# Performance work log

Hardware: AMD Instinct MI355X
Metric: run time of the kernel (lower is better)

## Reference

```python
import jax, jax.numpy as jnp
import numpy as np

ENC, TAG, LANG, ATT = 512, 512, 512, 256
N, P = 1024, 1024


def setup_inputs() -> dict:
    key = jax.random.key(0)
    ks = jax.random.split(key, 11)
    s = lambda d: 1.0 / np.sqrt(d)
    return {
        "encoder_out": jax.random.normal(ks[0], (1, P, ENC), jnp.float32),
        "decoder_hidden": jax.random.normal(ks[1], (N, TAG), jnp.float32),
        "language_out": jax.random.normal(ks[2], (N, LANG), jnp.float32),
        "We": jax.random.uniform(ks[3], (ATT, ENC), jnp.float32, -s(ENC), s(ENC)),
        "be": jax.random.uniform(ks[4], (ATT,), jnp.float32, -s(ENC), s(ENC)),
        "Wt": jax.random.uniform(ks[5], (ATT, TAG), jnp.float32, -s(TAG), s(TAG)),
        "bt": jax.random.uniform(ks[6], (ATT,), jnp.float32, -s(TAG), s(TAG)),
        "Wl": jax.random.uniform(ks[7], (ATT, LANG), jnp.float32, -s(LANG), s(LANG)),
        "bl": jax.random.uniform(ks[8], (ATT,), jnp.float32, -s(LANG), s(LANG)),
        "Wf": jax.random.uniform(ks[9], (1, ATT), jnp.float32, -s(ATT), s(ATT)),
        "bf": jax.random.uniform(ks[10], (1,), jnp.float32, -s(ATT), s(ATT)),
    }


def reference(encoder_out, decoder_hidden, language_out, We, be, Wt, bt, Wl, bl, Wf, bf):
    # att1: (1, P, A); att2, att3: (N, A)
    att1 = jnp.einsum("bpe,ae->bpa", encoder_out, We) + be
    att2 = decoder_hidden @ Wt.T + bt
    att3 = language_out @ Wl.T + bl
    # broadcast add -> (N, P, A), relu, reduce to scalar score per pixel
    h = jax.nn.relu(att1 + (att2 + att3)[:, None, :])  # (N, P, A)
    att = jnp.einsum("npa,a->np", h, Wf[0]) + bf[0]     # (N, P)
    alpha = jax.nn.softmax(att, axis=1)
    # softmax-weighted sum over pixels -> (N, ENC)
    awe = jnp.einsum("np,pe->ne", alpha, encoder_out[0])
    return awe, alpha
```

## Files before the change

### kernel.cpp

```cpp
#include <hip/hip_runtime.h>
#include <hip/hip_bf16.h>
#include <math.h>

#define ENC 512
#define ATT 256
#define NN 1024
#define PP 1024

typedef __attribute__((ext_vector_type(8))) __bf16 bf16x8;
typedef __attribute__((ext_vector_type(4))) float floatx4;
typedef __attribute__((ext_vector_type(2))) float floatx2;

union LdsVec { uint4 u; bf16x8 v; };

__device__ __forceinline__ unsigned cvt_pk(float lo, float hi) {
    union { __hip_bfloat162 h; unsigned u; } x;
    x.h = __float22bfloat162_rn(float2{lo, hi});
    return x.u;
}
__device__ __forceinline__ uint4 cvt8(float4 f0, float4 f1) {
    uint4 r;
    r.x = cvt_pk(f0.x, f0.y); r.y = cvt_pk(f0.z, f0.w);
    r.z = cvt_pk(f1.x, f1.y); r.w = cvt_pk(f1.z, f1.w);
    return r;
}

__device__ __forceinline__ int tile_off(int row, int k) {
    return row * 32 + ((((k >> 3) ^ ((row >> 1) & 3)) & 3) << 3) + (k & 7);
}

__device__ __forceinline__ void stage_bt(unsigned short* dst, const float* __restrict__ src,
                                         int ld, int k0, int tid) {
    const int row = tid >> 2, kseg = tid & 3;
    const float* p = src + (size_t)row * ld + k0 + kseg * 8;
    float4 f0 = *(const float4*)p;
    float4 f1 = *(const float4*)(p + 4);
    uint4 u = cvt8(f0, f1);
    *(uint4*)&dst[tile_off(row, kseg * 8)] = u;
}

__global__ __launch_bounds__(256) void mfma_uv(
    const float* __restrict__ E,  const float* __restrict__ We, const float* __restrict__ be,
    const float* __restrict__ D,  const float* __restrict__ Wt, const float* __restrict__ bt,
    const float* __restrict__ Lg, const float* __restrict__ Wl, const float* __restrict__ bl,
    float* __restrict__ uT, float* __restrict__ v1T, float* __restrict__ v2T,
    unsigned short* __restrict__ ET)
{
    const int tid = threadIdx.x;

    if (blockIdx.z == 3) {
        __shared__ unsigned short T[64][72];
        const int k0 = blockIdx.y * 64;
        const int kr = tid >> 2, nc = (tid & 3) * 16;
        const int nr = tid >> 2, kc = (tid & 3) * 16;
        #pragma unroll
        for (int t = 0; t < 2; ++t) {
            const int n0 = (blockIdx.x * 2 + t) * 64;
            const float* ep = E + (size_t)(k0 + kr) * ENC + n0 + nc;
            float4 a = *(const float4*)(ep + 0),  b = *(const float4*)(ep + 4);
            float4 c = *(const float4*)(ep + 8),  d = *(const float4*)(ep + 12);
            if (t) __syncthreads();
            *(uint4*)&T[kr][nc]     = cvt8(a, b);
            *(uint4*)&T[kr][nc + 8] = cvt8(c, d);
            __syncthreads();
            unsigned short tmp[16];
            #pragma unroll
            for (int i = 0; i < 16; ++i) tmp[i] = T[kc + i][nr];
            unsigned short* op = ET + (size_t)(n0 + nr) * PP + k0 + kc;
            *(uint4*)(op)     = *(uint4*)&tmp[0];
            *(uint4*)(op + 8) = *(uint4*)&tmp[8];
        }
        return;
    }

    __shared__ __align__(16) unsigned short As[2][64 * 32];
    __shared__ __align__(16) unsigned short Bs[2][64 * 32];
    const int K = 512;

    const float *A, *B, *bias; float* out;
    if      (blockIdx.z == 0) { A = E;  B = We; bias = be; out = uT;  }
    else if (blockIdx.z == 1) { A = D;  B = Wt; bias = bt; out = v1T; }
    else                      { A = Lg; B = Wl; bias = bl; out = v2T; }

    const int m0 = blockIdx.y * 64, n0 = blockIdx.x * 64;
    const int wv = tid >> 6, lm = tid & 15, lq = (tid >> 4) & 3;
    const int mb = (wv & 1) * 32, nb = (wv >> 1) * 32;
    const int a0o = tile_off(mb + lm,      lq * 8);
    const int a1o = tile_off(mb + 16 + lm, lq * 8);
    const int b0o = tile_off(nb + lm,      lq * 8);
    const int b1o = tile_off(nb + 16 + lm, lq * 8);

    const int row = tid >> 2, kseg = tid & 3;
    const int soff = tile_off(row, kseg * 8);
    const float* Ap = A + (size_t)(m0 + row) * K + kseg * 8;
    const float* Bp = B + (size_t)(n0 + row) * K + kseg * 8;

    floatx4 acc[2][2];
    const floatx4 zero = {0.f, 0.f, 0.f, 0.f};
    acc[0][0] = zero; acc[0][1] = zero; acc[1][0] = zero; acc[1][1] = zero;

    float4 pa0 = *(const float4*)(Ap), pa1 = *(const float4*)(Ap + 4);
    float4 pb0 = *(const float4*)(Bp), pb1 = *(const float4*)(Bp + 4);

    for (int k0 = 0; k0 < K; k0 += 32) {
        const int buf = (k0 >> 5) & 1;
        *(uint4*)&As[buf][soff] = cvt8(pa0, pa1);
        *(uint4*)&Bs[buf][soff] = cvt8(pb0, pb1);
        __syncthreads();
        if (k0 + 32 < K) {
            pa0 = *(const float4*)(Ap + k0 + 32); pa1 = *(const float4*)(Ap + k0 + 36);
            pb0 = *(const float4*)(Bp + k0 + 32); pb1 = *(const float4*)(Bp + k0 + 36);
        }
        LdsVec fa0, fa1, fb0, fb1;
        fa0.u = *(const uint4*)&As[buf][a0o];
        fa1.u = *(const uint4*)&As[buf][a1o];
        fb0.u = *(const uint4*)&Bs[buf][b0o];
        fb1.u = *(const uint4*)&Bs[buf][b1o];
        acc[0][0] = __builtin_amdgcn_mfma_f32_16x16x32_bf16(fa0.v, fb0.v, acc[0][0], 0, 0, 0);
        acc[0][1] = __builtin_amdgcn_mfma_f32_16x16x32_bf16(fa0.v, fb1.v, acc[0][1], 0, 0, 0);
        acc[1][0] = __builtin_amdgcn_mfma_f32_16x16x32_bf16(fa1.v, fb0.v, acc[1][0], 0, 0, 0);
        acc[1][1] = __builtin_amdgcn_mfma_f32_16x16x32_bf16(fa1.v, fb1.v, acc[1][1], 0, 0, 0);
    }

    #pragma unroll
    for (int s = 0; s < 2; ++s) {
        const int col = n0 + nb + s * 16 + lm;
        const float bsum = bias[col];
        #pragma unroll
        for (int t = 0; t < 2; ++t) {
            const int mbase = m0 + mb + t * 16 + lq * 4;
            float4 o;
            o.x = acc[t][s][0] + bsum; o.y = acc[t][s][1] + bsum;
            o.z = acc[t][s][2] + bsum; o.w = acc[t][s][3] + bsum;
            *(float4*)&out[(size_t)col * NN + mbase] = o;
        }
    }
}

__global__ __launch_bounds__(256) void att_fused(
    const float* __restrict__ uT, const float* __restrict__ v1T,
    const float* __restrict__ v2T,
    const float* __restrict__ Wf, float* __restrict__ att_part)
{
    __shared__ float us[32][68];
    __shared__ float vs[32][68];
    __shared__ float wfs[128];
    const int tid = threadIdx.x;
    const int z = blockIdx.z;
    if (tid < 128) wfs[tid] = Wf[z * 128 + tid];
    const int p0 = blockIdx.x * 64, n0 = blockIdx.y * 64;
    const int rowS = tid >> 3, cS = (tid & 7) * 8;
    const int tx = tid & 15, ty = tid >> 4;

    floatx2 acc[4][2];
    const floatx2 z2 = {0.f, 0.f};
    #pragma unroll
    for (int j = 0; j < 4; ++j) { acc[j][0] = z2; acc[j][1] = z2; }

    const int abase = z * 128;
    for (int ac = 0; ac < 128; ac += 32) {
        __syncthreads();
        {
            const float* up = &uT[(size_t)(abase + ac + rowS) * NN + p0 + cS];
            float4 f0 = *(const float4*)up;
            float4 f1 = *(const float4*)(up + 4);
            *(float4*)&us[rowS][cS]     = f0;
            *(float4*)&us[rowS][cS + 4] = f1;
            const size_t vidx = (size_t)(abase + ac + rowS) * NN + n0 + cS;
            float4 g0 = *(const float4*)&v1T[vidx];
            float4 g1 = *(const float4*)&v1T[vidx + 4];
            float4 h0 = *(const float4*)&v2T[vidx];
            float4 h1 = *(const float4*)&v2T[vidx + 4];
            float4 s0, s1;
            s0.x = g0.x + h0.x; s0.y = g0.y + h0.y; s0.z = g0.z + h0.z; s0.w = g0.w + h0.w;
            s1.x = g1.x + h1.x; s1.y = g1.y + h1.y; s1.z = g1.z + h1.z; s1.w = g1.w + h1.w;
            *(float4*)&vs[rowS][cS]     = s0;
            *(float4*)&vs[rowS][cS + 4] = s1;
        }
        __syncthreads();
        #pragma unroll
        for (int a4 = 0; a4 < 32; a4 += 4) {
            float4 w4 = *(const float4*)&wfs[ac + a4];
            #pragma unroll
            for (int aa = 0; aa < 4; ++aa) {
                const int a = a4 + aa;
                float4 u4 = *(const float4*)&us[a][tx * 4];
                float4 v4 = *(const float4*)&vs[a][ty * 4];
                const float w = (aa == 0) ? w4.x : (aa == 1) ? w4.y : (aa == 2) ? w4.z : w4.w;
                floatx2 ulo = {u4.x, u4.y}, uhi = {u4.z, u4.w};
                const float vv[4] = {v4.x, v4.y, v4.z, v4.w};
                #pragma unroll
                for (int j = 0; j < 4; ++j) {
                    floatx2 t0 = ulo + vv[j];
                    floatx2 t1 = uhi + vv[j];
                    t0 = __builtin_elementwise_max(t0, z2);
                    t1 = __builtin_elementwise_max(t1, z2);
                    acc[j][0] = t0 * w + acc[j][0];
                    acc[j][1] = t1 * w + acc[j][1];
                }
            }
        }
    }

    float* outp = att_part + (size_t)z * NN * PP;
    #pragma unroll
    for (int j = 0; j < 4; ++j) {
        float4 o;
        o.x = acc[j][0].x; o.y = acc[j][0].y; o.z = acc[j][1].x; o.w = acc[j][1].y;
        *(float4*)&outp[(size_t)(n0 + ty * 4 + j) * PP + p0 + tx * 4] = o;
    }
}

__global__ __launch_bounds__(256) void softmax_rows(
    const float* __restrict__ att_part, float* __restrict__ alpha,
    unsigned short* __restrict__ alpha_bf)
{
    const int wv = threadIdx.x >> 6, lane = threadIdx.x & 63;
    const int n = blockIdx.x * 4 + wv;
    const float* r0 = att_part + (size_t)n * PP;
    const float* r1 = att_part + (size_t)NN * PP + (size_t)n * PP;

    float4 x[4];
    #pragma unroll
    for (int i = 0; i < 4; ++i) {
        float4 a = *(const float4*)&r0[i * 256 + lane * 4];
        float4 b = *(const float4*)&r1[i * 256 + lane * 4];
        x[i].x = a.x + b.x; x[i].y = a.y + b.y; x[i].z = a.z + b.z; x[i].w = a.w + b.w;
    }

    float m = -1e30f;
    #pragma unroll
    for (int i = 0; i < 4; ++i)
        m = fmaxf(m, fmaxf(fmaxf(x[i].x, x[i].y), fmaxf(x[i].z, x[i].w)));
    #pragma unroll
    for (int off = 32; off > 0; off >>= 1) m = fmaxf(m, __shfl_xor(m, off, 64));

    float s = 0.f;
    #pragma unroll
    for (int i = 0; i < 4; ++i) {
        x[i].x = __expf(x[i].x - m); x[i].y = __expf(x[i].y - m);
        x[i].z = __expf(x[i].z - m); x[i].w = __expf(x[i].w - m);
        s += x[i].x + x[i].y + x[i].z + x[i].w;
    }
    #pragma unroll
    for (int off = 32; off > 0; off >>= 1) s += __shfl_xor(s, off, 64);
    const float inv = 1.0f / s;

    float* ar = alpha + (size_t)n * PP;
    unsigned short* br = alpha_bf + (size_t)n * PP;
    #pragma unroll
    for (int i = 0; i < 4; ++i) {
        x[i].x *= inv; x[i].y *= inv; x[i].z *= inv; x[i].w *= inv;
        *(float4*)&ar[i * 256 + lane * 4] = x[i];
        uint2 pk;
        pk.x = cvt_pk(x[i].x, x[i].y);
        pk.y = cvt_pk(x[i].z, x[i].w);
        *(uint2*)&br[i * 256 + lane * 4] = pk;
    }
}

__global__ __launch_bounds__(256) void mfma_awe(
    const unsigned short* __restrict__ alpha_bf,
    const unsigned short* __restrict__ ET, float* __restrict__ awe)
{
    __shared__ __align__(16) unsigned short As[2][32 * 32];
    __shared__ __align__(16) unsigned short Bs[2][64 * 32];
    const int tid = threadIdx.x;
    const int K = PP;
    const int m0 = blockIdx.y * 32, n0 = blockIdx.x * 64;
    const int wv = tid >> 6, lm = tid & 15, lq = (tid >> 4) & 3;
    const int mw = (wv & 1) * 16, nw = (wv >> 1) * 32;
    const int a0o = tile_off(mw + lm,      lq * 8);
    const int b0o = tile_off(nw + lm,      lq * 8);
    const int b1o = tile_off(nw + 16 + lm, lq * 8);

    const int rowA = tid >> 3, kcA = (tid & 7) * 4;
    const int rowB = tid >> 2, kcB = (tid & 3) * 8;
    const int aoff = tile_off(rowA, kcA);
    const int boff = tile_off(rowB, kcB);
    const unsigned short* Ap = alpha_bf + (size_t)(m0 + rowA) * PP + kcA;
    const unsigned short* Bp = ET + (size_t)(n0 + rowB) * PP + kcB;

    floatx4 acc[2];
    const floatx4 zero = {0.f, 0.f, 0.f, 0.f};
    acc[0] = zero; acc[1] = zero;

    uint2 pa = *(const uint2*)Ap;
    uint4 pb = *(const uint4*)Bp;

    for (int k0 = 0; k0 < K; k0 += 32) {
        const int buf = (k0 >> 5) & 1;
        *(uint2*)&As[buf][aoff] = pa;
        *(uint4*)&Bs[buf][boff] = pb;
        __syncthreads();
        if (k0 + 32 < K) {
            pa = *(const uint2*)(Ap + k0 + 32);
            pb = *(const uint4*)(Bp + k0 + 32);
        }
        LdsVec fa, fb0, fb1;
        fa.u  = *(const uint4*)&As[buf][a0o];
        fb0.u = *(const uint4*)&Bs[buf][b0o];
        fb1.u = *(const uint4*)&Bs[buf][b1o];
        acc[0] = __builtin_amdgcn_mfma_f32_16x16x32_bf16(fa.v, fb0.v, acc[0], 0, 0, 0);
        acc[1] = __builtin_amdgcn_mfma_f32_16x16x32_bf16(fa.v, fb1.v, acc[1], 0, 0, 0);
    }

    #pragma unroll
    for (int s = 0; s < 2; ++s) {
        const int col = n0 + nw + s * 16 + lm;
        #pragma unroll
        for (int r = 0; r < 4; ++r)
            awe[(size_t)(m0 + mw + lq * 4 + r) * ENC + col] = acc[s][r];
    }
}

extern "C" void kernel_launch(void* const* d_in, const int* in_sizes, int n_in,
                              void* d_out, int out_size, void* d_ws, size_t ws_size,
                              hipStream_t stream)
{
    const float* encoder = (const float*)d_in[0];
    const float* dec     = (const float*)d_in[1];
    const float* lang    = (const float*)d_in[2];
    const float* We      = (const float*)d_in[3];
    const float* be      = (const float*)d_in[4];
    const float* Wt      = (const float*)d_in[5];
    const float* bt      = (const float*)d_in[6];
    const float* Wl      = (const float*)d_in[7];
    const float* bl      = (const float*)d_in[8];
    const float* Wf      = (const float*)d_in[9];

    float* uT   = (float*)d_ws;
    float* v1T  = uT  + ATT * NN;
    float* v2T  = v1T + ATT * NN;
    float* attp = v2T + ATT * NN;
    unsigned short* alpha_bf = (unsigned short*)(attp + 2 * (size_t)NN * PP);
    unsigned short* ET       = alpha_bf + (size_t)NN * PP;

    float* awe   = (float*)d_out;
    float* alpha = (float*)d_out + NN * ENC;

    mfma_uv<<<dim3(4, 16, 4), 256, 0, stream>>>(
        encoder, We, be, dec, Wt, bt, lang, Wl, bl, uT, v1T, v2T, ET);
    att_fused<<<dim3(PP / 64, NN / 64, 2), 256, 0, stream>>>(uT, v1T, v2T, Wf, attp);
    softmax_rows<<<dim3(NN / 4), 256, 0, stream>>>(attp, alpha, alpha_bf);
    mfma_awe<<<dim3(ENC / 64, NN / 32), 256, 0, stream>>>(alpha_bf, ET, awe);
}
```

Before: 126.1 us.

## Store projections as bf16 and widen att_fused tile to 128 pixels

After: 127.2 us. About the same (+0.9%).

```diff
diff --git a/kernel.cpp b/kernel.cpp
--- a/kernel.cpp
+++ b/kernel.cpp
@@ -24,27 +24,22 @@
     r.z = cvt_pk(f1.x, f1.y); r.w = cvt_pk(f1.z, f1.w);
     return r;
 }
+__device__ __forceinline__ float2 bfpair(unsigned w) {
+    union { unsigned u; float f; } lo, hi;
+    lo.u = w << 16; hi.u = w & 0xffff0000u;
+    return float2{lo.f, hi.f};
+}
 
 __device__ __forceinline__ int tile_off(int row, int k) {
     return row * 32 + ((((k >> 3) ^ ((row >> 1) & 3)) & 3) << 3) + (k & 7);
-}
-
-__device__ __forceinline__ void stage_bt(unsigned short* dst, const float* __restrict__ src,
-                                         int ld, int k0, int tid) {
-    const int row = tid >> 2, kseg = tid & 3;
-    const float* p = src + (size_t)row * ld + k0 + kseg * 8;
-    float4 f0 = *(const float4*)p;
-    float4 f1 = *(const float4*)(p + 4);
-    uint4 u = cvt8(f0, f1);
-    *(uint4*)&dst[tile_off(row, kseg * 8)] = u;
 }
 
 __global__ __launch_bounds__(256) void mfma_uv(
     const float* __restrict__ E,  const float* __restrict__ We, const float* __restrict__ be,
     const float* __restrict__ D,  const float* __restrict__ Wt, const float* __restrict__ bt,
     const float* __restrict__ Lg, const float* __restrict__ Wl, const float* __restrict__ bl,
-    float* __restrict__ uT, float* __restrict__ v1T, float* __restrict__ v2T,
-    unsigned short* __restrict__ ET)
+    unsigned short* __restrict__ uT, unsigned short* __restrict__ v1T,
+    unsigned short* __restrict__ v2T, unsigned short* __restrict__ ET)
 {
     const int tid = threadIdx.x;
 
@@ -77,7 +72,7 @@
     __shared__ __align__(16) unsigned short Bs[2][64 * 32];
     const int K = 512;
 
-    const float *A, *B, *bias; float* out;
+    const float *A, *B, *bias; unsigned short* out;
     if      (blockIdx.z == 0) { A = E;  B = We; bias = be; out = uT;  }
     else if (blockIdx.z == 1) { A = D;  B = Wt; bias = bt; out = v1T; }
     else                      { A = Lg; B = Wl; bias = bl; out = v2T; }
@@ -129,75 +124,84 @@
         #pragma unroll
         for (int t = 0; t < 2; ++t) {
             const int mbase = m0 + mb + t * 16 + lq * 4;
-            float4 o;
-            o.x = acc[t][s][0] + bsum; o.y = acc[t][s][1] + bsum;
-            o.z = acc[t][s][2] + bsum; o.w = acc[t][s][3] + bsum;
-            *(float4*)&out[(size_t)col * NN + mbase] = o;
+            uint2 o;
+            o.x = cvt_pk(acc[t][s][0] + bsum, acc[t][s][1] + bsum);
+            o.y = cvt_pk(acc[t][s][2] + bsum, acc[t][s][3] + bsum);
+            *(uint2*)&out[(size_t)col * NN + mbase] = o;
         }
     }
 }
 
 __global__ __launch_bounds__(256) void att_fused(
-    const float* __restrict__ uT, const float* __restrict__ v1T,
-    const float* __restrict__ v2T,
+    const unsigned short* __restrict__ uT, const unsigned short* __restrict__ v1T,
+    const unsigned short* __restrict__ v2T,
     const float* __restrict__ Wf, float* __restrict__ att_part)
 {
-    __shared__ float us[32][68];
+    __shared__ float us[32][132];
     __shared__ float vs[32][68];
     __shared__ float wfs[128];
     const int tid = threadIdx.x;
     const int z = blockIdx.z;
     if (tid < 128) wfs[tid] = Wf[z * 128 + tid];
-    const int p0 = blockIdx.x * 64, n0 = blockIdx.y * 64;
-    const int rowS = tid >> 3, cS = (tid & 7) * 8;
+    const int p0 = blockIdx.x * 128, n0 = blockIdx.y * 64;
+    const int arow = tid >> 3, t8 = tid & 7;
+    const int pcol = t8 * 16, ncol = t8 * 8;
     const int tx = tid & 15, ty = tid >> 4;
 
-    floatx2 acc[4][2];
+    floatx2 acc[4][4];
     const floatx2 z2 = {0.f, 0.f};
     #pragma unroll
-    for (int j = 0; j < 4; ++j) { acc[j][0] = z2; acc[j][1] = z2; }
+    for (int j = 0; j < 4; ++j)
+        #pragma unroll
+        for (int h = 0; h < 4; ++h) acc[j][h] = z2;
 
     const int abase = z * 128;
     for (int ac = 0; ac < 128; ac += 32) {
         __syncthreads();
         {
-            const float* up = &uT[(size_t)(abase + ac + rowS) * NN + p0 + cS];
-            float4 f0 = *(const float4*)up;
-            float4 f1 = *(const float4*)(up + 4);
-            *(float4*)&us[rowS][cS]     = f0;
-            *(float4*)&us[rowS][cS + 4] = f1;
-            const size_t vidx = (size_t)(abase + ac + rowS) * NN + n0 + cS;
-            float4 g0 = *(const float4*)&v1T[vidx];
-            float4 g1 = *(const float4*)&v1T[vidx + 4];
-            float4 h0 = *(const float4*)&v2T[vidx];
-            float4 h1 = *(const float4*)&v2T[vidx + 4];
-            float4 s0, s1;
-            s0.x = g0.x + h0.x; s0.y = g0.y + h0.y; s0.z = g0.z + h0.z; s0.w = g0.w + h0.w;
-            s1.x = g1.x + h1.x; s1.y = g1.y + h1.y; s1.z = g1.z + h1.z; s1.w = g1.w + h1.w;
-            *(float4*)&vs[rowS][cS]     = s0;
-            *(float4*)&vs[rowS][cS + 4] = s1;
+            const size_t arow_g = (size_t)(abase + ac + arow) * NN;
+            const unsigned short* up = uT + arow_g + p0 + pcol;
+            uint4 ua = *(const uint4*)up;
+            uint4 ub = *(const uint4*)(up + 8);
+            float* ud = &us[arow][pcol];
+            float2 c;
+            c = bfpair(ua.x); ud[0] = c.x; ud[1] = c.y;
+            c = bfpair(ua.y); ud[2] = c.x; ud[3] = c.y;
+            c = bfpair(ua.z); ud[4] = c.x; ud[5] = c.y;
+            c = bfpair(ua.w); ud[6] = c.x; ud[7] = c.y;
+            c = bfpair(ub.x); ud[8] = c.x; ud[9] = c.y;
+            c = bfpair(ub.y); ud[10] = c.x; ud[11] = c.y;
+            c = bfpair(ub.z); ud[12] = c.x; ud[13] = c.y;
+            c = bfpair(ub.w); ud[14] = c.x; ud[15] = c.y;
+            uint4 va = *(const uint4*)(v1T + arow_g + n0 + ncol);
+            uint4 vb = *(const uint4*)(v2T + arow_g + n0 + ncol);
+            float* vd = &vs[arow][ncol];
+            float2 a0, b0;
+            a0 = bfpair(va.x); b0 = bfpair(vb.x); vd[0] = a0.x + b0.x; vd[1] = a0.y + b0.y;
+            a0 = bfpair(va.y); b0 = bfpair(vb.y); vd[2] = a0.x + b0.x; vd[3] = a0.y + b0.y;
+            a0 = bfpair(va.z); b0 = bfpair(vb.z); vd[4] = a0.x + b0.x; vd[5] = a0.y + b0.y;
+            a0 = bfpair(va.w); b0 = bfpair(vb.w); vd[6] = a0.x + b0.x; vd[7] = a0.y + b0.y;
         }
         __syncthreads();
         #pragma unroll
-        for (int a4 = 0; a4 < 32; a4 += 4) {
-            float4 w4 = *(const float4*)&wfs[ac + a4];
+        for (int a = 0; a < 32; ++a) {
+            float4 u0 = *(const float4*)&us[a][tx * 4];
+            float4 u1 = *(const float4*)&us[a][tx * 4 + 64];
+            float4 v4 = *(const float4*)&vs[a][ty * 4];
+            const float w = wfs[ac + a];
+            floatx2 u00 = {u0.x, u0.y}, u01 = {u0.z, u0.w};
+            floatx2 u10 = {u1.x, u1.y}, u11 = {u1.z, u1.w};
+            const float vv[4] = {v4.x, v4.y, v4.z, v4.w};
             #pragma unroll
-            for (int aa = 0; aa < 4; ++aa) {
-                const int a = a4 + aa;
-                float4 u4 = *(const float4*)&us[a][tx * 4];
-                float4 v4 = *(const float4*)&vs[a][ty * 4];
-                const float w = (aa == 0) ? w4.x : (aa == 1) ? w4.y : (aa == 2) ? w4.z : w4.w;
-                floatx2 ulo = {u4.x, u4.y}, uhi = {u4.z, u4.w};
-                const float vv[4] = {v4.x, v4.y, v4.z, v4.w};
-                #pragma unroll
-                for (int j = 0; j < 4; ++j) {
-                    floatx2 t0 = ulo + vv[j];
-                    floatx2 t1 = uhi + vv[j];
-                    t0 = __builtin_elementwise_max(t0, z2);
-                    t1 = __builtin_elementwise_max(t1, z2);
-                    acc[j][0] = t0 * w + acc[j][0];
-                    acc[j][1] = t1 * w + acc[j][1];
-                }
+            for (int j = 0; j < 4; ++j) {
+                floatx2 t0 = __builtin_elementwise_max(u00 + vv[j], z2);
+                floatx2 t1 = __builtin_elementwise_max(u01 + vv[j], z2);
+                floatx2 t2 = __builtin_elementwise_max(u10 + vv[j], z2);
+                floatx2 t3 = __builtin_elementwise_max(u11 + vv[j], z2);
+                acc[j][0] = t0 * w + acc[j][0];
+                acc[j][1] = t1 * w + acc[j][1];
+                acc[j][2] = t2 * w + acc[j][2];
+                acc[j][3] = t3 * w + acc[j][3];
             }
         }
     }
@@ -205,9 +209,12 @@
     float* outp = att_part + (size_t)z * NN * PP;
     #pragma unroll
     for (int j = 0; j < 4; ++j) {
+        float* rowp = &outp[(size_t)(n0 + ty * 4 + j) * PP + p0];
         float4 o;
         o.x = acc[j][0].x; o.y = acc[j][0].y; o.z = acc[j][1].x; o.w = acc[j][1].y;
-        *(float4*)&outp[(size_t)(n0 + ty * 4 + j) * PP + p0 + tx * 4] = o;
+        *(float4*)&rowp[tx * 4] = o;
+        o.x = acc[j][2].x; o.y = acc[j][2].y; o.z = acc[j][3].x; o.w = acc[j][3].y;
+        *(float4*)&rowp[tx * 4 + 64] = o;
     }
 }
 
@@ -329,10 +336,10 @@
     const float* bl      = (const float*)d_in[8];
     const float* Wf      = (const float*)d_in[9];
 
-    float* uT   = (float*)d_ws;
-    float* v1T  = uT  + ATT * NN;
-    float* v2T  = v1T + ATT * NN;
-    float* attp = v2T + ATT * NN;
+    unsigned short* uT  = (unsigned short*)d_ws;
+    unsigned short* v1T = uT  + ATT * NN;
+    unsigned short* v2T = v1T + ATT * NN;
+    float* attp = (float*)(v2T + ATT * NN);
     unsigned short* alpha_bf = (unsigned short*)(attp + 2 * (size_t)NN * PP);
     unsigned short* ET       = alpha_bf + (size_t)NN * PP;
 
@@ -341,7 +348,7 @@
 
     mfma_uv<<<dim3(4, 16, 4), 256, 0, stream>>>(
         encoder, We, be, dec, Wt, bt, lang, Wl, bl, uT, v1T, v2T, ET);
-    att_fused<<<dim3(PP / 64, NN / 64, 2), 256, 0, stream>>>(uT, v1T, v2T, Wf, attp);
+    att_fused<<<dim3(PP / 128, NN / 64, 2), 256, 0, stream>>>(uT, v1T, v2T, Wf, attp);
     softmax_rows<<<dim3(NN / 4), 256, 0, stream>>>(attp, alpha, alpha_bf);
     mfma_awe<<<dim3(ENC / 64, NN / 32), 256, 0, stream>>>(alpha_bf, ET, awe);
 }
```
